# Kernel tuning notes

Hardware: AMD Instinct MI355X
Metric: run time of the kernel (lower is better)

The kernel has to match this reference:

```python
import jax, jax.numpy as jnp
import numpy as np

NETS = 32
NODES = [256, 512, 512, 128]
BATCH = 4096


def setup_inputs() -> dict:
    key = jax.random.key(0)
    ks = jax.random.split(key, 7)
    def lin_init(k, n_out, n_in):
        # mimic nn.Linear default init scale
        bound = 1.0 / np.sqrt(n_in)
        kw, kb = jax.random.split(k)
        W = jax.random.uniform(kw, (NETS, n_out, n_in), jnp.float32, -bound, bound)
        b = jax.random.uniform(kb, (NETS, n_out), jnp.float32, -bound, bound)
        return W, b
    x = jax.random.normal(ks[0], (BATCH, NODES[0]), jnp.float32)
    W1, b1 = lin_init(ks[1], NODES[1], NODES[0])
    W2, b2 = lin_init(ks[2], NODES[2], NODES[1])
    W3, b3 = lin_init(ks[3], NODES[3], NODES[2])
    return {"x": x, "W1": W1, "b1": b1, "W2": W2, "b2": b2, "W3": W3, "b3": b3}


def reference(x, W1, b1, W2, b2, W3, b3):
    # Ensemble of independent MLPs expressed as batched GEMMs over the `nets` axis.
    # x: [B, in]; Wl: [N, out_l, in_l]; bl: [N, out_l]
    h = jax.nn.relu(jnp.einsum('bi,noi->bno', x, W1) + b1)        # [B, N, 512]
    h = jax.nn.relu(jnp.einsum('bni,noi->bno', h, W2) + b2)       # [B, N, 512]
    out = jnp.einsum('bni,noi->bno', h, W3) + b3                  # [B, N, 128] (identity act)
    B = x.shape[0]
    # Concatenate per-net outputs along feature dim: y[:, n*out_len:(n+1)*out_len]
    return out.reshape(B, -1)
```

## Files before the change

kernel.cpp:

```cpp
#include <hip/hip_runtime.h>

#define NETS 32
#define BATCH 4096
#define D0 256
#define D1 512
#define D2 512
#define D3 128
#define MT 64
#define LDA (D0 + 8)
#define LDH (D1 + 8)
#define LDO 132

using half8 = __attribute__((ext_vector_type(8))) _Float16;
using half4 = __attribute__((ext_vector_type(4))) _Float16;
using f32x4 = __attribute__((ext_vector_type(4))) float;

#define W1_N (NETS * D1 * D0)
#define W2_N (NETS * D2 * D1)
#define W3_N (NETS * D3 * D2)

__global__ void cvt_weights(const float* __restrict__ W1, const float* __restrict__ W2,
                            const float* __restrict__ W3,
                            _Float16* __restrict__ W1h, _Float16* __restrict__ W2h,
                            _Float16* __restrict__ W3h) {
    const int i = blockIdx.x * blockDim.x + threadIdx.x;
    constexpr int T1 = W1_N / 8, T2 = W2_N / 8, T3 = W3_N / 8;
    const float* src;
    _Float16* dstf;
    int l;
    if (i < T1) {
        int u = i; l = u & 63; int f = u >> 6;
        int ni = f & 3, kk = (f >> 2) & 7;
        int netw = f >> 5;
        int w = netw & 7, net = netw >> 3;
        int n = w * 64 + ni * 16 + (l >> 2);
        int k = kk * 32 + (l & 3) * 8;
        src = W1 + (size_t)net * D1 * D0 + (size_t)n * D0 + k;
        dstf = W1h + (size_t)f * 512;
    } else if (i < T1 + T2) {
        int u = i - T1; l = u & 63; int f = u >> 6;
        int ni = f & 3, kk = (f >> 2) & 15;
        int netw = f >> 6;
        int w = netw & 7, net = netw >> 3;
        int n = w * 64 + ni * 16 + (l >> 2);
        int k = kk * 32 + (l & 3) * 8;
        src = W2 + (size_t)net * D2 * D1 + (size_t)n * D1 + k;
        dstf = W2h + (size_t)f * 512;
    } else {
        int u = i - T1 - T2; l = u & 63; int f = u >> 6;
        int kk = f & 15;
        int netw = f >> 4;
        int w = netw & 7, net = netw >> 3;
        int n = w * 16 + (l >> 2);
        int k = kk * 32 + (l & 3) * 8;
        src = W3 + (size_t)net * D3 * D2 + (size_t)n * D2 + k;
        dstf = W3h + (size_t)f * 512;
    }
    float4 v0 = *reinterpret_cast<const float4*>(src);
    float4 v1 = *reinterpret_cast<const float4*>(src + 4);
    half8 o;
    o[0] = (_Float16)v0.x; o[1] = (_Float16)v0.y; o[2] = (_Float16)v0.z; o[3] = (_Float16)v0.w;
    o[4] = (_Float16)v1.x; o[5] = (_Float16)v1.y; o[6] = (_Float16)v1.z; o[7] = (_Float16)v1.w;
    const int lp = ((l & 3) << 4) | (l >> 2);
    *reinterpret_cast<half8*>(dstf + lp * 8) = o;
}

template<int K, int NI, int G, int MI>
__device__ __forceinline__ void layer_mfma(const _Float16* As, int lda,
                                           const _Float16* __restrict__ wl,
                                           int lane16, int quad,
                                           f32x4 (&acc)[MI][NI]) {
    constexpr int NFR = (K / 32) * NI;
    constexpr int STEPS = NFR / G;
    half8 bcur[G], bnxt[G];
    half8 a[MI];
#pragma unroll
    for (int g = 0; g < G; ++g)
        bcur[g] = *reinterpret_cast<const half8*>(wl + (size_t)g * 512);
#pragma unroll
    for (int s = 0; s < STEPS; ++s) {
        const int fb = s * G;
        if (s + 1 < STEPS) {
#pragma unroll
            for (int g = 0; g < G; ++g)
                bnxt[g] = *reinterpret_cast<const half8*>(wl + (size_t)(fb + G + g) * 512);
        }
        if (fb % NI == 0) {
            const int kk = fb / NI;
#pragma unroll
            for (int mi = 0; mi < MI; ++mi)
                a[mi] = *reinterpret_cast<const half8*>(
                    As + (mi * 16 + lane16) * lda + kk * 32 + quad * 8);
        }
#pragma unroll
        for (int g = 0; g < G; ++g) {
            const int ni = (fb + g) % NI;
#pragma unroll
            for (int mi = 0; mi < MI; ++mi)
                acc[mi][ni] = __builtin_amdgcn_mfma_f32_16x16x32_f16(a[mi], bcur[g], acc[mi][ni], 0, 0, 0);
        }
        if (s + 1 < STEPS) {
#pragma unroll
            for (int g = 0; g < G; ++g) bcur[g] = bnxt[g];
        }
    }
}

template<int MI, int NI>
__device__ __forceinline__ void store_act(f32x4 (&acc)[MI][NI], const float* __restrict__ bias,
                                          _Float16* dst, int ldd, int n_base,
                                          int lane16, int quad) {
#pragma unroll
    for (int ni = 0; ni < NI; ++ni) {
        float bv = bias[n_base + ni * 16 + lane16];
        int col = n_base + ni * 16 + lane16;
#pragma unroll
        for (int mi = 0; mi < MI; ++mi) {
#pragma unroll
            for (int r = 0; r < 4; ++r) {
                float v = acc[mi][ni][r] + bv;
                v = fmaxf(v, 0.0f);
                int row = mi * 16 + quad * 4 + r;
                dst[row * ldd + col] = (_Float16)v;
            }
        }
    }
}

__global__ __launch_bounds__(512, 4) void mlp_fused(
    const float* __restrict__ X,
    const _Float16* __restrict__ W1h, const float* __restrict__ b1,
    const _Float16* __restrict__ W2h, const float* __restrict__ b2,
    const _Float16* __restrict__ W3h, const float* __restrict__ b3,
    float* __restrict__ out) {
    __shared__ __align__(16) _Float16 buf[MT * LDH];

    const int tid = threadIdx.x;
    const int w = tid >> 6;
    const int l = tid & 63;
    const int lane16 = l & 15;
    const int quad = l >> 4;

    const int bb = blockIdx.x;
    const int xcd = bb & 7;
    const int s = bb >> 3;
    const int net = xcd * 4 + (s >> 6);
    const int mt = s & 63;
    const int m0 = mt * MT;

    {
        const float* xsrc = X + (size_t)m0 * D0;
#pragma unroll
        for (int it = 0; it < 8; ++it) {
            int chunk = it * 512 + tid;
            int row = chunk >> 6;
            int c4 = chunk & 63;
            float4 v = *reinterpret_cast<const float4*>(xsrc + row * D0 + c4 * 4);
            half4 o;
            o[0] = (_Float16)v.x; o[1] = (_Float16)v.y;
            o[2] = (_Float16)v.z; o[3] = (_Float16)v.w;
            *reinterpret_cast<half4*>(&buf[row * LDA + c4 * 4]) = o;
        }
    }
    __syncthreads();

    {
        f32x4 acc[4][4] = {};
        const _Float16* wl = W1h + ((size_t)(net * 8 + w) * 32) * 512 + l * 8;
        layer_mfma<D0, 4, 4, 4>(buf, LDA, wl, lane16, quad, acc);
        __syncthreads();
        store_act<4, 4>(acc, b1 + net * D1, buf, LDH, w * 64, lane16, quad);
    }
    __syncthreads();

    {
        f32x4 acc[4][4] = {};
        const _Float16* wl = W2h + ((size_t)(net * 8 + w) * 64) * 512 + l * 8;
        layer_mfma<D1, 4, 4, 4>(buf, LDH, wl, lane16, quad, acc);
        __syncthreads();
        store_act<4, 4>(acc, b2 + net * D2, buf, LDH, w * 64, lane16, quad);
    }
    __syncthreads();

    {
        f32x4 acc[4][1] = {};
        const _Float16* wl = W3h + ((size_t)(net * 8 + w) * 16) * 512 + l * 8;
        layer_mfma<D2, 1, 1, 4>(buf, LDH, wl, lane16, quad, acc);
        __syncthreads();
        float* buff = reinterpret_cast<float*>(buf);
        const int n_base = w * 16;
        const float bv = b3[net * D3 + n_base + lane16];
#pragma unroll
        for (int mi = 0; mi < 4; ++mi) {
#pragma unroll
            for (int r = 0; r < 4; ++r) {
                int row = mi * 16 + quad * 4 + r;
                buff[row * LDO + n_base + lane16] = acc[mi][0][r] + bv;
            }
        }
        __syncthreads();
#pragma unroll
        for (int it = 0; it < 4; ++it) {
            int idx = it * 512 + tid;
            int row = idx >> 5;
            int c4 = idx & 31;
            f32x4 v = *reinterpret_cast<const f32x4*>(&buff[row * LDO + c4 * 4]);
            *reinterpret_cast<f32x4*>(
                &out[(size_t)(m0 + row) * (NETS * D3) + net * D3 + c4 * 4]) = v;
        }
    }
}

extern "C" void kernel_launch(void* const* d_in, const int* in_sizes, int n_in,
                              void* d_out, int out_size, void* d_ws, size_t ws_size,
                              hipStream_t stream) {
    const float* x  = (const float*)d_in[0];
    const float* W1 = (const float*)d_in[1];
    const float* b1 = (const float*)d_in[2];
    const float* W2 = (const float*)d_in[3];
    const float* b2 = (const float*)d_in[4];
    const float* W3 = (const float*)d_in[5];
    const float* b3 = (const float*)d_in[6];
    float* out = (float*)d_out;

    _Float16* W1h = (_Float16*)d_ws;
    _Float16* W2h = W1h + (size_t)W1_N;
    _Float16* W3h = W2h + (size_t)W2_N;

    const int totalT = (W1_N + W2_N + W3_N) / 8;
    cvt_weights<<<totalT / 256, 256, 0, stream>>>(W1, W2, W3, W1h, W2h, W3h);

    mlp_fused<<<NETS * (BATCH / MT), 512, 0, stream>>>(x, W1h, b1, W2h, b2, W3h, b3, out);
}
```

Baseline: 270.4 us.

## Double batch tile to 128 rows with 1024-thread blocks and unswizzled fp16 weights

Raises the batch tile per block from 64 to 128 rows and uses 16 waves per block, so each fp16 weight fragment is reused across twice as many rows and total weight traffic from global memory halves. Waves now cover 32 output columns with 8 M-fragments each, and layer 3 splits waves into row-halves by column groups. The weight conversion kernel drops its MFMA-fragment swizzle and writes plain row-major fp16, so the GEMM loop reads per-lane strided rows, which coalesces less well. The larger LDS footprint, fewer blocks, and a 1024-thread launch bound with high accumulator pressure risk lower occupancy or register spills.

```diff
diff --git a/kernel.cpp b/kernel.cpp
--- a/kernel.cpp
+++ b/kernel.cpp
@@ -6,7 +6,7 @@
 #define D1 512
 #define D2 512
 #define D3 128
-#define MT 64
+#define MT 128
 #define LDA (D0 + 8)
 #define LDH (D1 + 8)
 #define LDO 132
@@ -19,71 +19,52 @@
 #define W2_N (NETS * D2 * D1)
 #define W3_N (NETS * D3 * D2)
 
-__global__ void cvt_weights(const float* __restrict__ W1, const float* __restrict__ W2,
-                            const float* __restrict__ W3,
-                            _Float16* __restrict__ W1h, _Float16* __restrict__ W2h,
-                            _Float16* __restrict__ W3h) {
+__global__ __launch_bounds__(256) void cvt_weights(
+    const float* __restrict__ W1, const float* __restrict__ W2,
+    const float* __restrict__ W3,
+    _Float16* __restrict__ W1h, _Float16* __restrict__ W2h,
+    _Float16* __restrict__ W3h) {
     const int i = blockIdx.x * blockDim.x + threadIdx.x;
-    constexpr int T1 = W1_N / 8, T2 = W2_N / 8, T3 = W3_N / 8;
+    constexpr int T1 = W1_N / 8, T2 = W2_N / 8;
     const float* src;
-    _Float16* dstf;
-    int l;
-    if (i < T1) {
-        int u = i; l = u & 63; int f = u >> 6;
-        int ni = f & 3, kk = (f >> 2) & 7;
-        int netw = f >> 5;
-        int w = netw & 7, net = netw >> 3;
-        int n = w * 64 + ni * 16 + (l >> 2);
-        int k = kk * 32 + (l & 3) * 8;
-        src = W1 + (size_t)net * D1 * D0 + (size_t)n * D0 + k;
-        dstf = W1h + (size_t)f * 512;
-    } else if (i < T1 + T2) {
-        int u = i - T1; l = u & 63; int f = u >> 6;
-        int ni = f & 3, kk = (f >> 2) & 15;
-        int netw = f >> 6;
-        int w = netw & 7, net = netw >> 3;
-        int n = w * 64 + ni * 16 + (l >> 2);
-        int k = kk * 32 + (l & 3) * 8;
-        src = W2 + (size_t)net * D2 * D1 + (size_t)n * D1 + k;
-        dstf = W2h + (size_t)f * 512;
-    } else {
-        int u = i - T1 - T2; l = u & 63; int f = u >> 6;
-        int kk = f & 15;
-        int netw = f >> 4;
-        int w = netw & 7, net = netw >> 3;
-        int n = w * 16 + (l >> 2);
-        int k = kk * 32 + (l & 3) * 8;
-        src = W3 + (size_t)net * D3 * D2 + (size_t)n * D2 + k;
-        dstf = W3h + (size_t)f * 512;
-    }
-    float4 v0 = *reinterpret_cast<const float4*>(src);
-    float4 v1 = *reinterpret_cast<const float4*>(src + 4);
+    _Float16* dst;
+    if (i < T1)           { src = W1 + (size_t)i * 8;            dst = W1h + (size_t)i * 8; }
+    else if (i < T1 + T2) { size_t u = (size_t)(i - T1) * 8;      src = W2 + u; dst = W2h + u; }
+    else                  { size_t u = (size_t)(i - T1 - T2) * 8; src = W3 + u; dst = W3h + u; }
+    f32x4 v0 = *reinterpret_cast<const f32x4*>(src);
+    f32x4 v1 = *reinterpret_cast<const f32x4*>(src + 4);
     half8 o;
-    o[0] = (_Float16)v0.x; o[1] = (_Float16)v0.y; o[2] = (_Float16)v0.z; o[3] = (_Float16)v0.w;
-    o[4] = (_Float16)v1.x; o[5] = (_Float16)v1.y; o[6] = (_Float16)v1.z; o[7] = (_Float16)v1.w;
-    const int lp = ((l & 3) << 4) | (l >> 2);
-    *reinterpret_cast<half8*>(dstf + lp * 8) = o;
+    o[0] = (_Float16)v0[0]; o[1] = (_Float16)v0[1]; o[2] = (_Float16)v0[2]; o[3] = (_Float16)v0[3];
+    o[4] = (_Float16)v1[0]; o[5] = (_Float16)v1[1]; o[6] = (_Float16)v1[2]; o[7] = (_Float16)v1[3];
+    *reinterpret_cast<half8*>(dst) = o;
 }
 
 template<int K, int NI, int G, int MI>
 __device__ __forceinline__ void layer_mfma(const _Float16* As, int lda,
-                                           const _Float16* __restrict__ wl,
+                                           const _Float16* __restrict__ wlane,
                                            int lane16, int quad,
                                            f32x4 (&acc)[MI][NI]) {
-    constexpr int NFR = (K / 32) * NI;
+    constexpr int KK = K / 32;
+    constexpr int NFR = KK * NI;
     constexpr int STEPS = NFR / G;
+    static_assert(G <= NI || NI == 1, "step must stay within one kk");
     half8 bcur[G], bnxt[G];
     half8 a[MI];
 #pragma unroll
-    for (int g = 0; g < G; ++g)
-        bcur[g] = *reinterpret_cast<const half8*>(wl + (size_t)g * 512);
+    for (int g = 0; g < G; ++g) {
+        const int kk = g / NI, ni = g % NI;
+        bcur[g] = *reinterpret_cast<const half8*>(wlane + (size_t)ni * 16 * K + kk * 32);
+    }
 #pragma unroll
     for (int s = 0; s < STEPS; ++s) {
         const int fb = s * G;
         if (s + 1 < STEPS) {
 #pragma unroll
-            for (int g = 0; g < G; ++g)
-                bnxt[g] = *reinterpret_cast<const half8*>(wl + (size_t)(fb + G + g) * 512);
+            for (int g = 0; g < G; ++g) {
+                const int f = fb + G + g;
+                const int kk = f / NI, ni = f % NI;
+                bnxt[g] = *reinterpret_cast<const half8*>(wlane + (size_t)ni * 16 * K + kk * 32);
+            }
         }
         if (fb % NI == 0) {
             const int kk = fb / NI;
@@ -127,7 +108,7 @@
     }
 }
 
-__global__ __launch_bounds__(512, 4) void mlp_fused(
+__global__ __launch_bounds__(1024, 4) void mlp_fused(
     const float* __restrict__ X,
     const _Float16* __restrict__ W1h, const float* __restrict__ b1,
     const _Float16* __restrict__ W2h, const float* __restrict__ b2,
@@ -144,15 +125,15 @@
     const int bb = blockIdx.x;
     const int xcd = bb & 7;
     const int s = bb >> 3;
-    const int net = xcd * 4 + (s >> 6);
-    const int mt = s & 63;
+    const int net = xcd * 4 + (s >> 5);
+    const int mt = s & 31;
     const int m0 = mt * MT;
 
     {
         const float* xsrc = X + (size_t)m0 * D0;
 #pragma unroll
         for (int it = 0; it < 8; ++it) {
-            int chunk = it * 512 + tid;
+            int chunk = it * 1024 + tid;
             int row = chunk >> 6;
             int c4 = chunk & 63;
             float4 v = *reinterpret_cast<const float4*>(xsrc + row * D0 + c4 * 4);
@@ -165,43 +146,44 @@
     __syncthreads();
 
     {
-        f32x4 acc[4][4] = {};
-        const _Float16* wl = W1h + ((size_t)(net * 8 + w) * 32) * 512 + l * 8;
-        layer_mfma<D0, 4, 4, 4>(buf, LDA, wl, lane16, quad, acc);
-        __syncthreads();
-        store_act<4, 4>(acc, b1 + net * D1, buf, LDH, w * 64, lane16, quad);
+        f32x4 acc[8][2] = {};
+        const _Float16* wlane = W1h + (size_t)net * D1 * D0 + (size_t)(w * 32 + lane16) * D0 + quad * 8;
+        layer_mfma<D0, 2, 2, 8>(buf, LDA, wlane, lane16, quad, acc);
+        __syncthreads();
+        store_act<8, 2>(acc, b1 + net * D1, buf, LDH, w * 32, lane16, quad);
     }
     __syncthreads();
 
     {
-        f32x4 acc[4][4] = {};
-        const _Float16* wl = W2h + ((size_t)(net * 8 + w) * 64) * 512 + l * 8;
-        layer_mfma<D1, 4, 4, 4>(buf, LDH, wl, lane16, quad, acc);
-        __syncthreads();
-        store_act<4, 4>(acc, b2 + net * D2, buf, LDH, w * 64, lane16, quad);
+        f32x4 acc[8][2] = {};
+        const _Float16* wlane = W2h + (size_t)net * D2 * D1 + (size_t)(w * 32 + lane16) * D1 + quad * 8;
+        layer_mfma<D1, 2, 2, 8>(buf, LDH, wlane, lane16, quad, acc);
+        __syncthreads();
+        store_act<8, 2>(acc, b2 + net * D2, buf, LDH, w * 32, lane16, quad);
     }
     __syncthreads();
 
     {
+        const int wr = w >> 3, wc = w & 7;
         f32x4 acc[4][1] = {};
-        const _Float16* wl = W3h + ((size_t)(net * 8 + w) * 16) * 512 + l * 8;
-        layer_mfma<D2, 1, 1, 4>(buf, LDH, wl, lane16, quad, acc);
+        const _Float16* wlane = W3h + (size_t)net * D3 * D2 + (size_t)(wc * 16 + lane16) * D2 + quad * 8;
+        layer_mfma<D2, 1, 1, 4>(buf + wr * 64 * LDH, LDH, wlane, lane16, quad, acc);
         __syncthreads();
         float* buff = reinterpret_cast<float*>(buf);
-        const int n_base = w * 16;
-        const float bv = b3[net * D3 + n_base + lane16];
+        const int n0 = wc * 16;
+        const float bv = b3[net * D3 + n0 + lane16];
 #pragma unroll
         for (int mi = 0; mi < 4; ++mi) {
 #pragma unroll
             for (int r = 0; r < 4; ++r) {
-                int row = mi * 16 + quad * 4 + r;
-                buff[row * LDO + n_base + lane16] = acc[mi][0][r] + bv;
+                int row = wr * 64 + mi * 16 + quad * 4 + r;
+                buff[row * LDO + n0 + lane16] = acc[mi][0][r] + bv;
             }
         }
         __syncthreads();
 #pragma unroll
         for (int it = 0; it < 4; ++it) {
-            int idx = it * 512 + tid;
+            int idx = it * 1024 + tid;
             int row = idx >> 5;
             int c4 = idx & 31;
             f32x4 v = *reinterpret_cast<const f32x4*>(&buff[row * LDO + c4 * 4]);
@@ -230,5 +212,5 @@
     const int totalT = (W1_N + W2_N + W3_N) / 8;
     cvt_weights<<<totalT / 256, 256, 0, stream>>>(W1, W2, W3, W1h, W2h, W3h);
 
-    mlp_fused<<<NETS * (BATCH / MT), 512, 0, stream>>>(x, W1h, b1, W2h, b2, W3h, b3, out);
-}
+    mlp_fused<<<NETS * (BATCH / MT), 1024, 0, stream>>>(x, W1h, b1, W2h, b2, W3h, b3, out);
+}
```

Measured after the change: 412.7 us. 52.6% more time.
